# Optimization experiments

Measured on AMD Instinct MI355X. Metric: run time of the kernel, lower is better.

Reference implementation:

```python
import math
import jax, jax.numpy as jnp
import numpy as np

V, D, A, H, FF, L, MD = 500, 512, 512, 8, 2048, 6, 512
HD = A // H
B, S, T = 32, 512, 128


def setup_inputs() -> dict:
    key = jax.random.key(0)
    ks = jax.random.split(key, 40)
    init = lambda k, shape: (jax.random.normal(k, shape, jnp.float32) * 0.02)
    inp = {
        'memory': jax.random.normal(ks[0], (B, S, MD), jnp.float32),
        'memory_lens': jax.random.randint(ks[1], (B,), S // 2, S + 1),
        'ys_in_pad': jax.random.randint(ks[2], (B, T), 0, V),
        'ys_in_lens': jax.random.randint(ks[3], (B,), T // 2, T + 1),
        'emb': init(ks[4], (V, D)),
        'w_out': init(ks[5], (D, V)),
        'b_out': jnp.zeros((V,), jnp.float32),
        # per-layer params stacked on leading L axis (consumed by lax.scan)
        'ln_sa_g': jnp.ones((L, D), jnp.float32), 'ln_sa_b': jnp.zeros((L, D), jnp.float32),
        'sa_wq': init(ks[6], (L, D, A)), 'sa_bq': init(ks[7], (L, A)),
        'sa_wk': init(ks[8], (L, D, A)), 'sa_bk': init(ks[9], (L, A)),
        'sa_wv': init(ks[10], (L, D, A)), 'sa_bv': init(ks[11], (L, A)),
        'sa_wo': init(ks[12], (L, A, D)), 'sa_bo': init(ks[13], (L, D)),
        'ln_ca_g': jnp.ones((L, D), jnp.float32), 'ln_ca_b': jnp.zeros((L, D), jnp.float32),
        'ca_wq': init(ks[14], (L, D, A)), 'ca_bq': init(ks[15], (L, A)),
        'ca_wk': init(ks[16], (L, MD, A)), 'ca_bk': init(ks[17], (L, A)),
        'ca_wv': init(ks[18], (L, MD, A)), 'ca_bv': init(ks[19], (L, A)),
        'ca_wo': init(ks[20], (L, A, D)), 'ca_bo': init(ks[21], (L, D)),
        'ln_ff_g': jnp.ones((L, D), jnp.float32), 'ln_ff_b': jnp.zeros((L, D), jnp.float32),
        'ff_w1': init(ks[22], (L, D, FF)), 'ff_b1': init(ks[23], (L, FF)),
        'ff_w2': init(ks[24], (L, FF, D)), 'ff_b2': init(ks[25], (L, D)),
    }
    return inp


def _layernorm(x, g, b, eps=1e-5):
    m = jnp.mean(x, axis=-1, keepdims=True)
    v = jnp.mean(jnp.square(x - m), axis=-1, keepdims=True)
    return (x - m) * jax.lax.rsqrt(v + eps) * g + b


def _mha(q_in, k_in, v_in, mask, wq, bq, wk, bk, wv, bv, wo, bo):
    # mask: True = disallowed. (B, T, S) for self-attn, (B, 1, S) for cross-attn.
    b_, tq, _ = q_in.shape
    ts = k_in.shape[1]
    q = (q_in @ wq + bq).reshape(b_, tq, H, HD).transpose(0, 2, 1, 3)
    k = (k_in @ wk + bk).reshape(b_, ts, H, HD).transpose(0, 2, 1, 3)
    v = (v_in @ wv + bv).reshape(b_, ts, H, HD).transpose(0, 2, 1, 3)
    s = jnp.einsum('bhtd,bhsd->bhts', q, k) / math.sqrt(HD)
    # penalize_abs_values_gt(limit=50, penalty=1e-4) is identity in the forward
    # pass (it only injects an auxiliary gradient during training).
    s = jnp.where(mask[:, None, :, :], -jnp.inf, s)
    a = jax.nn.softmax(s, axis=-1)  # dropout p=0.0 in this config
    o = jnp.einsum('bhts,bhsd->bhtd', a, v).transpose(0, 2, 1, 3).reshape(b_, tq, A)
    return o @ wo + bo


def _forward(memory, memory_lens, ys_in_pad, ys_in_lens, emb, w_out, b_out, layer_params):
    t = ys_in_pad.shape[1]
    # make_pad_mask | ~subsequent_mask  -> (B, T, T), True = masked
    pad = jnp.arange(t)[None, :] >= ys_in_lens[:, None]            # (B, T)
    causal = ~jnp.tril(jnp.ones((t, t), bool))                     # (T, T)
    tgt_mask = pad[:, None, :] | causal[None]                      # (B, T, T)
    mem_mask = (jnp.arange(memory.shape[1])[None, :] >= memory_lens[:, None])[:, None, :]

    # embedding + sinusoidal positional encoding (dropout in eval = identity)
    pos = jnp.arange(t, dtype=jnp.float32)[:, None]
    div = jnp.exp(jnp.arange(0, D, 2, dtype=jnp.float32) * (-math.log(10000.0) / D))
    pe = jnp.zeros((t, D), jnp.float32)
    pe = pe.at[:, 0::2].set(jnp.sin(pos * div)).at[:, 1::2].set(jnp.cos(pos * div))
    x = emb[ys_in_pad] * math.sqrt(D) + pe[None]

    def step(tgt, p):
        tn = _layernorm(tgt, p['ln_sa_g'], p['ln_sa_b'])
        tgt = tgt + _mha(tn, tn, tn, tgt_mask,
                         p['sa_wq'], p['sa_bq'], p['sa_wk'], p['sa_bk'],
                         p['sa_wv'], p['sa_bv'], p['sa_wo'], p['sa_bo'])
        tn = _layernorm(tgt, p['ln_ca_g'], p['ln_ca_b'])
        tgt = tgt + _mha(tn, memory, memory, mem_mask,
                         p['ca_wq'], p['ca_bq'], p['ca_wk'], p['ca_bk'],
                         p['ca_wv'], p['ca_bv'], p['ca_wo'], p['ca_bo'])
        tn = _layernorm(tgt, p['ln_ff_g'], p['ln_ff_b'])
        h = tn @ p['ff_w1'] + p['ff_b1']
        h = h * jax.nn.sigmoid(h)  # Swish
        tgt = tgt + h @ p['ff_w2'] + p['ff_b2']
        return tgt, None

    x, _ = jax.lax.scan(step, x, layer_params)
    return x @ w_out + b_out  # (B, T, V) logits


_LAYER_KEYS = ['ln_sa_g', 'ln_sa_b', 'sa_wq', 'sa_bq', 'sa_wk', 'sa_bk', 'sa_wv', 'sa_bv',
               'sa_wo', 'sa_bo', 'ln_ca_g', 'ln_ca_b', 'ca_wq', 'ca_bq', 'ca_wk', 'ca_bk',
               'ca_wv', 'ca_bv', 'ca_wo', 'ca_bo', 'ln_ff_g', 'ln_ff_b',
               'ff_w1', 'ff_b1', 'ff_w2', 'ff_b2']


def reference(memory, memory_lens, ys_in_pad, ys_in_lens, emb, w_out, b_out,
              ln_sa_g, ln_sa_b, sa_wq, sa_bq, sa_wk, sa_bk, sa_wv, sa_bv, sa_wo, sa_bo,
              ln_ca_g, ln_ca_b, ca_wq, ca_bq, ca_wk, ca_bk, ca_wv, ca_bv, ca_wo, ca_bo,
              ln_ff_g, ln_ff_b, ff_w1, ff_b1, ff_w2, ff_b2):
    loc = locals()
    layer_params = {k: loc[k] for k in _LAYER_KEYS}
    return _forward(memory, memory_lens, ys_in_pad, ys_in_lens, emb, w_out, b_out, layer_params)
```

## Files before the change

### kernel.cpp

```cpp
#include <hip/hip_runtime.h>
#include <hip/hip_bf16.h>
#include <hip/hip_fp16.h>

constexpr int Bc = 32, Sc = 512, Tc = 128, Dc = 512, Ac = 512, Hc = 8;
constexpr int HDc = 64, FFc = 2048, Lc = 6, Vc = 500;
constexpr int NTOK = Bc * Tc;
constexpr int NMEM = Bc * Sc;

typedef unsigned short u16;
typedef __attribute__((ext_vector_type(8))) short short8;
typedef __attribute__((ext_vector_type(4))) float f32x4;

__device__ __forceinline__ u16 bfc(float x) {
  __hip_bfloat16 h = __float2bfloat16(x);
  return *reinterpret_cast<u16*>(&h);
}

__device__ __forceinline__ void gload16(const void* g, void* l) {
  __builtin_amdgcn_global_load_lds(
      (const __attribute__((address_space(1))) unsigned int*)g,
      (__attribute__((address_space(3))) unsigned int*)l, 16, 0, 0);
}

__device__ __forceinline__ float wave_sum(float v) {
#pragma unroll
  for (int o = 32; o > 0; o >>= 1) v += __shfl_down(v, o);
  return v;
}
__device__ __forceinline__ float wave_max(float v) {
#pragma unroll
  for (int o = 32; o > 0; o >>= 1) v = fmaxf(v, __shfl_down(v, o));
  return v;
}

__global__ __launch_bounds__(256) void embed_pe_k(const int* __restrict__ ys,
                                                  const float* __restrict__ emb,
                                                  float* __restrict__ x) {
  int tok = blockIdx.x;
  int t = tok & (Tc - 1);
  int id = ys[tok];
  int j = threadIdx.x;
  int d0 = 2 * j;
  const float cdiv = -9.210340371976184f / (float)Dc;
  float div = expf((float)d0 * cdiv);
  float ang = (float)t * div;
  float pe0 = sinf(ang), pe1 = cosf(ang);
  const float sc = 22.627416997969522f;
  long base = (long)tok * Dc + d0;
  long ebase = (long)id * Dc + d0;
  x[base]     = emb[ebase]     * sc + pe0;
  x[base + 1] = emb[ebase + 1] * sc + pe1;
}

__global__ __launch_bounds__(256) void layernorm_k(const float* __restrict__ x,
                                                   const float* __restrict__ g,
                                                   const float* __restrict__ bta,
                                                   u16* __restrict__ out) {
  int row = blockIdx.x;
  int tid = threadIdx.x;
  const float* xr = x + (long)row * Dc;
  float2 xv = *(const float2*)(xr + tid * 2);
  __shared__ float red[4];
  float s = wave_sum(xv.x + xv.y);
  if ((tid & 63) == 0) red[tid >> 6] = s;
  __syncthreads();
  float mean = (red[0] + red[1] + red[2] + red[3]) * (1.0f / Dc);
  float dx0 = xv.x - mean, dx1 = xv.y - mean;
  __syncthreads();
  float s2 = wave_sum(dx0 * dx0 + dx1 * dx1);
  if ((tid & 63) == 0) red[tid >> 6] = s2;
  __syncthreads();
  float var = (red[0] + red[1] + red[2] + red[3]) * (1.0f / Dc);
  float rstd = rsqrtf(var + 1e-5f);
  ushort2 o;
  o.x = bfc(dx0 * rstd * g[2 * tid] + bta[2 * tid]);
  o.y = bfc(dx1 * rstd * g[2 * tid + 1] + bta[2 * tid + 1]);
  *(ushort2*)(out + (long)row * Dc + tid * 2) = o;
}

__global__ __launch_bounds__(256) void wtrans_k(const float* __restrict__ src,
                                                u16* __restrict__ dst,
                                                int K, int N, long srcStride, long dstStride) {
  int z = blockIdx.z;
  src += z * srcStride;
  dst += z * dstStride;
  __shared__ float t[32][33];
  int n0 = blockIdx.x * 32, k0 = blockIdx.y * 32;
  int tx = threadIdx.x & 31, ty = threadIdx.x >> 5;
#pragma unroll
  for (int i = 0; i < 4; i++) {
    int n = n0 + tx;
    t[ty + 8 * i][tx] = (n < N) ? src[(long)(k0 + ty + 8 * i) * N + n] : 0.0f;
  }
  __syncthreads();
#pragma unroll
  for (int i = 0; i < 4; i++) {
    dst[(long)(n0 + ty + 8 * i) * K + k0 + tx] = bfc(t[tx][ty + 8 * i]);
  }
}

__global__ __launch_bounds__(256) void f2b_k(const float* __restrict__ in,
                                             u16* __restrict__ out, long n) {
  long i = ((long)blockIdx.x * 256 + threadIdx.x) * 4;
  if (i >= n) return;
  float4 v = *(const float4*)(in + i);
  ushort4 o;
  o.x = bfc(v.x); o.y = bfc(v.y); o.z = bfc(v.z); o.w = bfc(v.w);
  *(ushort4*)(out + i) = o;
}

template <int BMW, int OMODE, bool BIAS, bool RES, bool SWISH, bool NCH>
__global__ __launch_bounds__(256) void mgemm_k(
    const u16* __restrict__ A, const u16* __restrict__ Bt,
    const float* __restrict__ bias0, const float* __restrict__ bias1,
    const float* __restrict__ bias2,
    void* __restrict__ Cv, const float* __restrict__ R,
    int N, int K, int lda, int ldb, int ldc, int nbi,
    long batAo, long batAi, long batBo, long batBi, long batCo, long batCi) {
  constexpr int BM = BMW * 32;
  int z = blockIdx.z;
  int bo = z / nbi, bi = z - bo * nbi;
  const u16* Ab = A + bo * batAo + bi * batAi;
  const u16* Bb = Bt + bo * batBo + bi * batBi;
  long coff = bo * batCo + bi * batCi;
  const float* bias = nullptr;
  if constexpr (BIAS) bias = (bi == 0) ? bias0 : ((bi == 1) ? bias1 : bias2);
  int m0 = blockIdx.y * BM, n0 = blockIdx.x * 128;

  __shared__ __align__(16) u16 As[2][BM * 32];
  __shared__ __align__(16) u16 Bs[2][128 * 32];

  int tid = threadIdx.x;
  int lane = tid & 63, wid = tid >> 6;
  int wm = wid >> 1, wn = wid & 1;
  int fr = lane & 15, grp = lane >> 4;

  f32x4 acc[BMW][4];
#pragma unroll
  for (int i = 0; i < BMW; i++)
#pragma unroll
    for (int j = 0; j < 4; j++) acc[i][j] = (f32x4){0.f, 0.f, 0.f, 0.f};

  const u16* ga = Ab + (long)(m0 + (tid >> 2)) * lda + ((tid & 3) << 3);
  const u16* gb = Bb + (long)(n0 + (tid >> 2)) * ldb + ((tid & 3) << 3);

  auto STAGE = [&](int buf, int kt) {
    u16* lA = &As[buf][tid * 8];
    u16* lB = &Bs[buf][tid * 8];
    gload16(ga + kt, lA);
    if constexpr (BM == 128) gload16(ga + kt + (long)64 * lda, lA + 2048);
    gload16(gb + kt, lB);
    gload16(gb + kt + (long)64 * ldb, lB + 2048);
  };

  auto COMPUTE = [&](int buf) {
    short8 av[BMW], bv[4];
#pragma unroll
    for (int i = 0; i < BMW; i++)
      av[i] = *(const short8*)&As[buf][(wm * BMW * 16 + i * 16 + fr) * 32 + grp * 8];
#pragma unroll
    for (int j = 0; j < 4; j++)
      bv[j] = *(const short8*)&Bs[buf][(wn * 64 + j * 16 + fr) * 32 + grp * 8];
#pragma unroll
    for (int i = 0; i < BMW; i++)
#pragma unroll
      for (int j = 0; j < 4; j++)
        acc[i][j] = __builtin_amdgcn_mfma_f32_16x16x32_bf16(av[i], bv[j], acc[i][j], 0, 0, 0);
  };

  STAGE(0, 0);
  __syncthreads();
  int cur = 0;
  for (int kt = 32; kt < K; kt += 32) {
    STAGE(cur ^ 1, kt);
    COMPUTE(cur);
    __syncthreads();
    cur ^= 1;
  }
  COMPUTE(cur);

  int rbase = m0 + wm * BMW * 16 + grp * 4;
  int cbase = n0 + wn * 64 + fr;
#pragma unroll
  for (int i = 0; i < BMW; i++) {
#pragma unroll
    for (int j = 0; j < 4; j++) {
      int col = cbase + j * 16;
      if (NCH && col >= N) continue;
      float bb = 0.0f;
      if constexpr (BIAS) bb = bias[col];
#pragma unroll
      for (int r = 0; r < 4; r++) {
        int row = rbase + i * 16 + r;
        float v = acc[i][j][r] + bb;
        long idx = coff + (long)row * ldc + col;
        if constexpr (RES) v += R[idx];
        if constexpr (SWISH) v = v / (1.0f + expf(-v));
        if constexpr (OMODE == 0) ((u16*)Cv)[idx] = bfc(v);
        else ((float*)Cv)[idx] = v;
      }
    }
  }
}

template <int SKV, int KVBLK, bool CAUSAL, int IQ>
__global__ __launch_bounds__(256) void fattn_k(
    const u16* __restrict__ Q, const u16* __restrict__ Kg, const u16* __restrict__ Vg,
    u16* __restrict__ O, const int* __restrict__ lens) {
  constexpr int NJ  = KVBLK / 16;
  constexpr int NKV = KVBLK / 32;
  constexpr int NT  = SKV / KVBLK;
  constexpr int KST = 72;
  constexpr int VST = KVBLK + 8;
  constexpr int WR  = 16 * IQ;
  constexpr int WGR = 64 * IQ;
  constexpr int CH  = KVBLK / 32;

  __shared__ __align__(16) u16 Ks[KVBLK * KST];
  __shared__ __align__(16) u16 Vs[64 * VST];
  __shared__ __align__(16) u16 Ps[WGR * VST];

  int bh = blockIdx.x; int b = bh >> 3, h = bh & 7;
  int row00 = blockIdx.y * WGR;
  int tid = threadIdx.x, lane = tid & 63, wid = tid >> 6;
  int fr = lane & 15, grp = lane >> 4;
  int len = lens[b];
  int row0w = row00 + wid * WR;

  short8 qa[IQ][2];
  {
    const u16* qp = Q + ((long)b * Tc + row0w + fr) * 512 + h * 64 + grp * 8;
#pragma unroll
    for (int i = 0; i < IQ; i++)
#pragma unroll
      for (int k2 = 0; k2 < 2; k2++)
        qa[i][k2] = *(const short8*)(qp + (long)i * 16 * 512 + k2 * 32);
  }

  float m_run[IQ][4], l_run[IQ][4];
  f32x4 acc_o[IQ][4];
#pragma unroll
  for (int i = 0; i < IQ; i++)
#pragma unroll
    for (int r = 0; r < 4; r++) { m_run[i][r] = -1e30f; l_run[i][r] = 0.0f; }
#pragma unroll
  for (int i = 0; i < IQ; i++)
#pragma unroll
    for (int j = 0; j < 4; j++) acc_o[i][j] = (f32x4){0.f, 0.f, 0.f, 0.f};

  const u16* Kbase = Kg + ((long)b * SKV) * 512 + h * 64;
  const u16* Vbase = Vg + ((long)b * SKV) * 512 + h * 64;

  int NTeff = NT;
  if constexpr (CAUSAL) NTeff = (row00 + WGR - 1) / KVBLK + 1;
  int lenT = (len + KVBLK - 1) / KVBLK;
  if (lenT < NTeff) NTeff = lenT;

  short8 kreg[CH], vreg[CH];
#pragma unroll
  for (int c = 0; c < CH; c++) {
    int idx = tid + 256 * c; int kv = idx >> 3, s = idx & 7;
    kreg[c] = *(const short8*)(Kbase + (long)kv * 512 + s * 8);
    vreg[c] = *(const short8*)(Vbase + (long)kv * 512 + s * 8);
  }

  for (int t = 0; t < NTeff; t++) {
    int kv0 = t * KVBLK;
    __syncthreads();
#pragma unroll
    for (int c = 0; c < CH; c++) {
      int idx = tid + 256 * c; int kv = idx >> 3, s = idx & 7;
      *(short8*)&Ks[kv * KST + s * 8] = kreg[c];
#pragma unroll
      for (int j = 0; j < 8; j++)
        Vs[(s * 8 + j) * VST + kv] = (u16)vreg[c][j];
    }
    __syncthreads();
    if (t + 1 < NTeff) {
      int kvn = kv0 + KVBLK;
#pragma unroll
      for (int c = 0; c < CH; c++) {
        int idx = tid + 256 * c; int kv = idx >> 3, s = idx & 7;
        kreg[c] = *(const short8*)(Kbase + (long)(kvn + kv) * 512 + s * 8);
        vreg[c] = *(const short8*)(Vbase + (long)(kvn + kv) * 512 + s * 8);
      }
    }

    int jmax = NJ;
    if constexpr (CAUSAL) {
      jmax = (row0w + WR - 1 - kv0) / 16 + 1;
      if (jmax > NJ) jmax = NJ;
    }

    f32x4 accs[IQ][NJ];
#pragma unroll
    for (int j = 0; j < NJ; j++) {
      if (CAUSAL && j >= jmax) continue;
      short8 bv0 = *(const short8*)&Ks[(j * 16 + fr) * KST + grp * 8];
      short8 bv1 = *(const short8*)&Ks[(j * 16 + fr) * KST + 32 + grp * 8];
#pragma unroll
      for (int i = 0; i < IQ; i++) {
        f32x4 a = __builtin_amdgcn_mfma_f32_16x16x32_bf16(qa[i][0], bv0, (f32x4){0.f,0.f,0.f,0.f}, 0, 0, 0);
        accs[i][j] = __builtin_amdgcn_mfma_f32_16x16x32_bf16(qa[i][1], bv1, a, 0, 0, 0);
      }
    }

    float alpha[IQ][4];
#pragma unroll
    for (int i = 0; i < IQ; i++) {
#pragma unroll
      for (int r = 0; r < 4; r++) {
        int qrow = row0w + i * 16 + grp * 4 + r;
        float vmax = -1e30f;
#pragma unroll
        for (int j = 0; j < NJ; j++) {
          if (CAUSAL && j >= jmax) continue;
          int kvb = kv0 + j * 16 + fr;
          float s = accs[i][j][r] * 0.125f;
          bool msk = (kvb >= len) || (CAUSAL && kvb > qrow);
          s = msk ? -1e30f : s;
          accs[i][j][r] = s;
          vmax = fmaxf(vmax, s);
        }
        vmax = fmaxf(vmax, __shfl_xor(vmax, 1));
        vmax = fmaxf(vmax, __shfl_xor(vmax, 2));
        vmax = fmaxf(vmax, __shfl_xor(vmax, 4));
        vmax = fmaxf(vmax, __shfl_xor(vmax, 8));
        float mn = fmaxf(m_run[i][r], vmax);
        float al = __expf(m_run[i][r] - mn);
        m_run[i][r] = mn;
        alpha[i][r] = al;
        float rs = 0.0f;
#pragma unroll
        for (int j = 0; j < NJ; j++) {
          if (CAUSAL && j >= jmax) continue;
          float p = __expf(accs[i][j][r] - mn);
          accs[i][j][r] = p;
          rs += p;
        }
        rs += __shfl_xor(rs, 1);
        rs += __shfl_xor(rs, 2);
        rs += __shfl_xor(rs, 4);
        rs += __shfl_xor(rs, 8);
        l_run[i][r] = l_run[i][r] * al + rs;
      }
    }

#pragma unroll
    for (int i = 0; i < IQ; i++)
#pragma unroll
      for (int j = 0; j < NJ; j++) {
        if (CAUSAL && j >= jmax) continue;
#pragma unroll
        for (int r = 0; r < 4; r++) {
          int prow = wid * WR + i * 16 + grp * 4 + r;
          Ps[prow * VST + j * 16 + fr] = bfc(accs[i][j][r]);
        }
      }

#pragma unroll
    for (int i = 0; i < IQ; i++)
#pragma unroll
      for (int jd = 0; jd < 4; jd++)
#pragma unroll
        for (int r = 0; r < 4; r++)
          acc_o[i][jd][r] *= alpha[i][r];

    int kvmax = NKV;
    if constexpr (CAUSAL) {
      kvmax = (row0w + WR - 1 - kv0) / 32 + 1;
      if (kvmax > NKV) kvmax = NKV;
    }
#pragma unroll
    for (int kk = 0; kk < NKV; kk++) {
      if (CAUSAL && kk >= kvmax) continue;
      short8 pa[IQ];
#pragma unroll
      for (int i = 0; i < IQ; i++)
        pa[i] = *(const short8*)&Ps[(wid * WR + i * 16 + fr) * VST + kk * 32 + grp * 8];
#pragma unroll
      for (int jd = 0; jd < 4; jd++) {
        short8 vb = *(const short8*)&Vs[(jd * 16 + fr) * VST + kk * 32 + grp * 8];
#pragma unroll
        for (int i = 0; i < IQ; i++)
          acc_o[i][jd] = __builtin_amdgcn_mfma_f32_16x16x32_bf16(pa[i], vb, acc_o[i][jd], 0, 0, 0);
      }
    }
  }

#pragma unroll
  for (int i = 0; i < IQ; i++) {
#pragma unroll
    for (int r = 0; r < 4; r++) {
      float inv = 1.0f / l_run[i][r];
      long tok = (long)b * Tc + row0w + i * 16 + grp * 4 + r;
#pragma unroll
      for (int jd = 0; jd < 4; jd++)
        O[tok * 512 + h * 64 + jd * 16 + fr] = bfc(acc_o[i][jd][r] * inv);
    }
  }
}

extern "C" void kernel_launch(void* const* d_in, const int* in_sizes, int n_in,
                              void* d_out, int out_size, void* d_ws, size_t ws_size,
                              hipStream_t stream) {
  const float* memory   = (const float*)d_in[0];
  const int*   mem_lens = (const int*)d_in[1];
  const int*   ys       = (const int*)d_in[2];
  const int*   ys_lens  = (const int*)d_in[3];
  const float* emb      = (const float*)d_in[4];
  const float* w_out    = (const float*)d_in[5];
  const float* b_out    = (const float*)d_in[6];
  const float* pp[26];
  for (int i = 0; i < 26; i++) pp[i] = (const float*)d_in[7 + i];

  constexpr long PLW = 4194304;
  constexpr long OFF_SAQ = 0, OFF_SAK = 262144, OFF_SAV = 524288, OFF_SAO = 786432,
                 OFF_CAQ = 1048576, OFF_CAK = 1310720, OFF_CAV = 1572864,
                 OFF_CAO = 1835008, OFF_FF1 = 2097152, OFF_FF2 = 3145728,
                 OFF_WOUT = 6 * PLW;
  u16*   Wt   = (u16*)d_ws;
  float* X    = (float*)(Wt + 25427968);
  u16*   TO   = (u16*)(X + 2097152);
  u16*   QKV  = TO + 2097152;
  u16*   memb = QKV + 3 * 2097152;
  u16*   Kb   = memb + 8388608;
  u16*   SCR  = Kb + 8388608;
  float* OUT  = (float*)d_out;

  auto WT = [&](const float* src, long dstoff, int K, int N, int Npad, int Lz,
                long srcStride, long dstStride) {
    dim3 g(Npad / 32, K / 32, Lz);
    wtrans_k<<<g, 256, 0, stream>>>(src, Wt + dstoff, K, N, srcStride, dstStride);
  };
  WT(pp[2],  OFF_SAQ, 512, 512, 512, Lc, 262144, PLW);
  WT(pp[4],  OFF_SAK, 512, 512, 512, Lc, 262144, PLW);
  WT(pp[6],  OFF_SAV, 512, 512, 512, Lc, 262144, PLW);
  WT(pp[8],  OFF_SAO, 512, 512, 512, Lc, 262144, PLW);
  WT(pp[12], OFF_CAQ, 512, 512, 512, Lc, 262144, PLW);
  WT(pp[14], OFF_CAK, 512, 512, 512, Lc, 262144, PLW);
  WT(pp[16], OFF_CAV, 512, 512, 512, Lc, 262144, PLW);
  WT(pp[18], OFF_CAO, 512, 512, 512, Lc, 262144, PLW);
  WT(pp[22], OFF_FF1, 512, 2048, 2048, Lc, 1048576, PLW);
  WT(pp[24], OFF_FF2, 2048, 512, 512, Lc, 1048576, PLW);
  WT(w_out,  OFF_WOUT, 512, 500, 512, 1, 0, 0);

  f2b_k<<<(NMEM * Dc / 4 + 255) / 256, 256, 0, stream>>>(memory, memb, (long)NMEM * Dc);
  embed_pe_k<<<NTOK, 256, 0, stream>>>(ys, emb, X);

  for (int l = 0; l < Lc; l++) {
    const u16* WtL = Wt + (long)l * PLW;

    layernorm_k<<<NTOK, 256, 0, stream>>>(X, pp[0] + (long)l * Dc, pp[1] + (long)l * Dc, TO);
    mgemm_k<4, 0, true, false, false, false><<<dim3(4, 32, 3), 256, 0, stream>>>(
        TO, WtL + OFF_SAQ, pp[3] + (long)l * Ac, pp[5] + (long)l * Ac, pp[7] + (long)l * Ac,
        QKV, nullptr, 512, 512, 512, 512, 512, 3, 0, 0, 0, 262144, 0, 2097152);
    fattn_k<128, 128, true, 2><<<dim3(256, 1), 256, 0, stream>>>(
        QKV, QKV + 2097152, QKV + 2 * 2097152, TO, ys_lens);
    mgemm_k<2, 1, true, true, false, false><<<dim3(4, 64, 1), 256, 0, stream>>>(
        TO, WtL + OFF_SAO, pp[9] + (long)l * Dc, nullptr, nullptr, X, X,
        512, 512, 512, 512, 512, 1, 0, 0, 0, 0, 0, 0);

    layernorm_k<<<NTOK, 256, 0, stream>>>(X, pp[10] + (long)l * Dc, pp[11] + (long)l * Dc, TO);
    mgemm_k<2, 0, true, false, false, false><<<dim3(4, 64, 1), 256, 0, stream>>>(
        TO, WtL + OFF_CAQ, pp[13] + (long)l * Ac, nullptr, nullptr, QKV, nullptr,
        512, 512, 512, 512, 512, 1, 0, 0, 0, 0, 0, 0);
    mgemm_k<4, 0, true, false, false, false><<<dim3(4, 128, 2), 256, 0, stream>>>(
        memb, WtL + OFF_CAK, pp[15] + (long)l * Ac, pp[17] + (long)l * Ac, nullptr,
        Kb, nullptr, 512, 512, 512, 512, 512, 2, 0, 0, 0, 262144, 0, 8388608);
    fattn_k<512, 64, false, 1><<<dim3(256, 2), 256, 0, stream>>>(
        QKV, Kb, SCR, TO, mem_lens);
    mgemm_k<2, 1, true, true, false, false><<<dim3(4, 64, 1), 256, 0, stream>>>(
        TO, WtL + OFF_CAO, pp[19] + (long)l * Dc, nullptr, nullptr, X, X,
        512, 512, 512, 512, 512, 1, 0, 0, 0, 0, 0, 0);

    layernorm_k<<<NTOK, 256, 0, stream>>>(X, pp[20] + (long)l * Dc, pp[21] + (long)l * Dc, TO);
    mgemm_k<4, 0, true, false, true, false><<<dim3(16, 32, 1), 256, 0, stream>>>(
        TO, WtL + OFF_FF1, pp[23] + (long)l * FFc, nullptr, nullptr, SCR, nullptr,
        2048, 512, 512, 512, 2048, 1, 0, 0, 0, 0, 0, 0);
    mgemm_k<2, 1, true, true, false, false><<<dim3(4, 64, 1), 256, 0, stream>>>(
        SCR, WtL + OFF_FF2, pp[25] + (long)l * Dc, nullptr, nullptr, X, X,
        512, 2048, 2048, 2048, 512, 1, 0, 0, 0, 0, 0, 0);
  }

  f2b_k<<<(NTOK * Dc / 4 + 255) / 256, 256, 0, stream>>>(X, TO, (long)NTOK * Dc);
  mgemm_k<2, 1, true, false, false, true><<<dim3(4, 64, 1), 256, 0, stream>>>(
      TO, Wt + OFF_WOUT, b_out, nullptr, nullptr, OUT, nullptr,
      500, 512, 512, 512, 500, 1, 0, 0, 0, 0, 0, 0);
}
```

Before: 1.252 ms.

## Skip padded memory rows in KV GEMM, remap blocks across XCDs, batch weight transposes

Several unrelated changes land together. The GEMM kernel remaps workgroup IDs so consecutive tiles share an XCD, and gains an MLEN mode that exits early for memory-row tiles past each batch's memory length in the cross-attention K/V projection. The eight 512x512 weight transposes are merged into one launch, the attention kernel raises wave priority around its MFMA loops, and the cross-attention KV block grows from 64 to 128. Skipped K/V rows are left unwritten, which assumes the attention kernel masks all positions beyond memory_lens.

```diff
diff --git a/kernel.cpp b/kernel.cpp
--- a/kernel.cpp
+++ b/kernel.cpp
@@ -99,6 +99,25 @@
   }
 }
 
+struct PtrPack8 { const float* p[8]; };
+__global__ __launch_bounds__(256) void wtrans8_k(PtrPack8 P, u16* __restrict__ Wt,
+                                                 long PLW) {
+  int z = blockIdx.z;
+  int widx = z / 6, l = z - widx * 6;
+  const float* src = P.p[widx] + (long)l * 262144;
+  u16* dst = Wt + (long)widx * 262144 + (long)l * PLW;
+  __shared__ float t[32][33];
+  int n0 = blockIdx.x * 32, k0 = blockIdx.y * 32;
+  int tx = threadIdx.x & 31, ty = threadIdx.x >> 5;
+#pragma unroll
+  for (int i = 0; i < 4; i++)
+    t[ty + 8 * i][tx] = src[(long)(k0 + ty + 8 * i) * 512 + n0 + tx];
+  __syncthreads();
+#pragma unroll
+  for (int i = 0; i < 4; i++)
+    dst[(long)(n0 + ty + 8 * i) * 512 + k0 + tx] = bfc(t[tx][ty + 8 * i]);
+}
+
 __global__ __launch_bounds__(256) void f2b_k(const float* __restrict__ in,
                                              u16* __restrict__ out, long n) {
   long i = ((long)blockIdx.x * 256 + threadIdx.x) * 4;
@@ -109,23 +128,37 @@
   *(ushort4*)(out + i) = o;
 }
 
-template <int BMW, int OMODE, bool BIAS, bool RES, bool SWISH, bool NCH>
+template <int BMW, int OMODE, bool BIAS, bool RES, bool SWISH, bool NCH, bool MLEN>
 __global__ __launch_bounds__(256) void mgemm_k(
     const u16* __restrict__ A, const u16* __restrict__ Bt,
     const float* __restrict__ bias0, const float* __restrict__ bias1,
     const float* __restrict__ bias2,
-    void* __restrict__ Cv, const float* __restrict__ R,
+    void* __restrict__ Cv, const float* __restrict__ R, const int* __restrict__ mlens,
     int N, int K, int lda, int ldb, int ldc, int nbi,
     long batAo, long batAi, long batBo, long batBi, long batCo, long batCi) {
   constexpr int BM = BMW * 32;
-  int z = blockIdx.z;
+
+  int gx = gridDim.x, gy = gridDim.y;
+  int nwg = gx * gy * gridDim.z;
+  int orig = blockIdx.x + gx * (blockIdx.y + gy * blockIdx.z);
+  int q = nwg >> 3, r = nwg & 7, xcd = orig & 7, off = orig >> 3;
+  int wgid = (xcd < r ? xcd * (q + 1) : r * (q + 1) + (xcd - r) * q) + off;
+  int bxi = wgid % gx; int tmp = wgid / gx;
+  int byi = tmp % gy;  int bzi = tmp / gy;
+
+  int z = bzi;
   int bo = z / nbi, bi = z - bo * nbi;
+  int m0 = byi * BM, n0 = bxi * 128;
+
+  if constexpr (MLEN) {
+    if ((m0 & 511) >= mlens[m0 >> 9]) return;
+  }
+
   const u16* Ab = A + bo * batAo + bi * batAi;
   const u16* Bb = Bt + bo * batBo + bi * batBi;
   long coff = bo * batCo + bi * batCi;
   const float* bias = nullptr;
   if constexpr (BIAS) bias = (bi == 0) ? bias0 : ((bi == 1) ? bias1 : bias2);
-  int m0 = blockIdx.y * BM, n0 = blockIdx.x * 128;
 
   __shared__ __align__(16) u16 As[2][BM * 32];
   __shared__ __align__(16) u16 Bs[2][128 * 32];
@@ -190,9 +223,9 @@
       float bb = 0.0f;
       if constexpr (BIAS) bb = bias[col];
 #pragma unroll
-      for (int r = 0; r < 4; r++) {
-        int row = rbase + i * 16 + r;
-        float v = acc[i][j][r] + bb;
+      for (int r2 = 0; r2 < 4; r2++) {
+        int row = rbase + i * 16 + r2;
+        float v = acc[i][j][r2] + bb;
         long idx = coff + (long)row * ldc + col;
         if constexpr (RES) v += R[idx];
         if constexpr (SWISH) v = v / (1.0f + expf(-v));
@@ -293,6 +326,7 @@
     }
 
     f32x4 accs[IQ][NJ];
+    __builtin_amdgcn_s_setprio(1);
 #pragma unroll
     for (int j = 0; j < NJ; j++) {
       if (CAUSAL && j >= jmax) continue;
@@ -304,6 +338,7 @@
         accs[i][j] = __builtin_amdgcn_mfma_f32_16x16x32_bf16(qa[i][1], bv1, a, 0, 0, 0);
       }
     }
+    __builtin_amdgcn_s_setprio(0);
 
     float alpha[IQ][4];
 #pragma unroll
@@ -371,6 +406,7 @@
       kvmax = (row0w + WR - 1 - kv0) / 32 + 1;
       if (kvmax > NKV) kvmax = NKV;
     }
+    __builtin_amdgcn_s_setprio(1);
 #pragma unroll
     for (int kk = 0; kk < NKV; kk++) {
       if (CAUSAL && kk >= kvmax) continue;
@@ -386,6 +422,7 @@
           acc_o[i][jd] = __builtin_amdgcn_mfma_f32_16x16x32_bf16(pa[i], vb, acc_o[i][jd], 0, 0, 0);
       }
     }
+    __builtin_amdgcn_s_setprio(0);
   }
 
 #pragma unroll
@@ -428,22 +465,13 @@
   u16*   SCR  = Kb + 8388608;
   float* OUT  = (float*)d_out;
 
-  auto WT = [&](const float* src, long dstoff, int K, int N, int Npad, int Lz,
-                long srcStride, long dstStride) {
-    dim3 g(Npad / 32, K / 32, Lz);
-    wtrans_k<<<g, 256, 0, stream>>>(src, Wt + dstoff, K, N, srcStride, dstStride);
-  };
-  WT(pp[2],  OFF_SAQ, 512, 512, 512, Lc, 262144, PLW);
-  WT(pp[4],  OFF_SAK, 512, 512, 512, Lc, 262144, PLW);
-  WT(pp[6],  OFF_SAV, 512, 512, 512, Lc, 262144, PLW);
-  WT(pp[8],  OFF_SAO, 512, 512, 512, Lc, 262144, PLW);
-  WT(pp[12], OFF_CAQ, 512, 512, 512, Lc, 262144, PLW);
-  WT(pp[14], OFF_CAK, 512, 512, 512, Lc, 262144, PLW);
-  WT(pp[16], OFF_CAV, 512, 512, 512, Lc, 262144, PLW);
-  WT(pp[18], OFF_CAO, 512, 512, 512, Lc, 262144, PLW);
-  WT(pp[22], OFF_FF1, 512, 2048, 2048, Lc, 1048576, PLW);
-  WT(pp[24], OFF_FF2, 2048, 512, 512, Lc, 1048576, PLW);
-  WT(w_out,  OFF_WOUT, 512, 500, 512, 1, 0, 0);
+  PtrPack8 P8;
+  P8.p[0] = pp[2];  P8.p[1] = pp[4];  P8.p[2] = pp[6];  P8.p[3] = pp[8];
+  P8.p[4] = pp[12]; P8.p[5] = pp[14]; P8.p[6] = pp[16]; P8.p[7] = pp[18];
+  wtrans8_k<<<dim3(16, 16, 48), 256, 0, stream>>>(P8, Wt, PLW);
+  wtrans_k<<<dim3(64, 16, Lc), 256, 0, stream>>>(pp[22], Wt + OFF_FF1, 512, 2048, 1048576, PLW);
+  wtrans_k<<<dim3(16, 64, Lc), 256, 0, stream>>>(pp[24], Wt + OFF_FF2, 2048, 512, 1048576, PLW);
+  wtrans_k<<<dim3(16, 16, 1), 256, 0, stream>>>(w_out, Wt + OFF_WOUT, 512, 500, 0, 0);
 
   f2b_k<<<(NMEM * Dc / 4 + 255) / 256, 256, 0, stream>>>(memory, memb, (long)NMEM * Dc);
   embed_pe_k<<<NTOK, 256, 0, stream>>>(ys, emb, X);
@@ -452,39 +480,39 @@
     const u16* WtL = Wt + (long)l * PLW;
 
     layernorm_k<<<NTOK, 256, 0, stream>>>(X, pp[0] + (long)l * Dc, pp[1] + (long)l * Dc, TO);
-    mgemm_k<4, 0, true, false, false, false><<<dim3(4, 32, 3), 256, 0, stream>>>(
+    mgemm_k<4, 0, true, false, false, false, false><<<dim3(4, 32, 3), 256, 0, stream>>>(
         TO, WtL + OFF_SAQ, pp[3] + (long)l * Ac, pp[5] + (long)l * Ac, pp[7] + (long)l * Ac,
-        QKV, nullptr, 512, 512, 512, 512, 512, 3, 0, 0, 0, 262144, 0, 2097152);
+        QKV, nullptr, nullptr, 512, 512, 512, 512, 512, 3, 0, 0, 0, 262144, 0, 2097152);
     fattn_k<128, 128, true, 2><<<dim3(256, 1), 256, 0, stream>>>(
         QKV, QKV + 2097152, QKV + 2 * 2097152, TO, ys_lens);
-    mgemm_k<2, 1, true, true, false, false><<<dim3(4, 64, 1), 256, 0, stream>>>(
-        TO, WtL + OFF_SAO, pp[9] + (long)l * Dc, nullptr, nullptr, X, X,
+    mgemm_k<2, 1, true, true, false, false, false><<<dim3(4, 64, 1), 256, 0, stream>>>(
+        TO, WtL + OFF_SAO, pp[9] + (long)l * Dc, nullptr, nullptr, X, X, nullptr,
         512, 512, 512, 512, 512, 1, 0, 0, 0, 0, 0, 0);
 
     layernorm_k<<<NTOK, 256, 0, stream>>>(X, pp[10] + (long)l * Dc, pp[11] + (long)l * Dc, TO);
-    mgemm_k<2, 0, true, false, false, false><<<dim3(4, 64, 1), 256, 0, stream>>>(
-        TO, WtL + OFF_CAQ, pp[13] + (long)l * Ac, nullptr, nullptr, QKV, nullptr,
+    mgemm_k<2, 0, true, false, false, false, false><<<dim3(4, 64, 1), 256, 0, stream>>>(
+        TO, WtL + OFF_CAQ, pp[13] + (long)l * Ac, nullptr, nullptr, QKV, nullptr, nullptr,
         512, 512, 512, 512, 512, 1, 0, 0, 0, 0, 0, 0);
-    mgemm_k<4, 0, true, false, false, false><<<dim3(4, 128, 2), 256, 0, stream>>>(
+    mgemm_k<4, 0, true, false, false, false, true><<<dim3(4, 128, 2), 256, 0, stream>>>(
         memb, WtL + OFF_CAK, pp[15] + (long)l * Ac, pp[17] + (long)l * Ac, nullptr,
-        Kb, nullptr, 512, 512, 512, 512, 512, 2, 0, 0, 0, 262144, 0, 8388608);
-    fattn_k<512, 64, false, 1><<<dim3(256, 2), 256, 0, stream>>>(
+        Kb, nullptr, mem_lens, 512, 512, 512, 512, 512, 2, 0, 0, 0, 262144, 0, 8388608);
+    fattn_k<512, 128, false, 1><<<dim3(256, 2), 256, 0, stream>>>(
         QKV, Kb, SCR, TO, mem_lens);
-    mgemm_k<2, 1, true, true, false, false><<<dim3(4, 64, 1), 256, 0, stream>>>(
-        TO, WtL + OFF_CAO, pp[19] + (long)l * Dc, nullptr, nullptr, X, X,
+    mgemm_k<2, 1, true, true, false, false, false><<<dim3(4, 64, 1), 256, 0, stream>>>(
+        TO, WtL + OFF_CAO, pp[19] + (long)l * Dc, nullptr, nullptr, X, X, nullptr,
         512, 512, 512, 512, 512, 1, 0, 0, 0, 0, 0, 0);
 
     layernorm_k<<<NTOK, 256, 0, stream>>>(X, pp[20] + (long)l * Dc, pp[21] + (long)l * Dc, TO);
-    mgemm_k<4, 0, true, false, true, false><<<dim3(16, 32, 1), 256, 0, stream>>>(
-        TO, WtL + OFF_FF1, pp[23] + (long)l * FFc, nullptr, nullptr, SCR, nullptr,
+    mgemm_k<4, 0, true, false, true, false, false><<<dim3(16, 32, 1), 256, 0, stream>>>(
+        TO, WtL + OFF_FF1, pp[23] + (long)l * FFc, nullptr, nullptr, SCR, nullptr, nullptr,
         2048, 512, 512, 512, 2048, 1, 0, 0, 0, 0, 0, 0);
-    mgemm_k<2, 1, true, true, false, false><<<dim3(4, 64, 1), 256, 0, stream>>>(
-        SCR, WtL + OFF_FF2, pp[25] + (long)l * Dc, nullptr, nullptr, X, X,
+    mgemm_k<2, 1, true, true, false, false, false><<<dim3(4, 64, 1), 256, 0, stream>>>(
+        SCR, WtL + OFF_FF2, pp[25] + (long)l * Dc, nullptr, nullptr, X, X, nullptr,
         512, 2048, 2048, 2048, 512, 1, 0, 0, 0, 0, 0, 0);
   }
 
   f2b_k<<<(NTOK * Dc / 4 + 255) / 256, 256, 0, stream>>>(X, TO, (long)NTOK * Dc);
-  mgemm_k<2, 1, true, false, false, true><<<dim3(4, 64, 1), 256, 0, stream>>>(
-      TO, Wt + OFF_WOUT, b_out, nullptr, nullptr, OUT, nullptr,
+  mgemm_k<2, 1, true, false, false, true, false><<<dim3(4, 64, 1), 256, 0, stream>>>(
+      TO, Wt + OFF_WOUT, b_out, nullptr, nullptr, OUT, nullptr, nullptr,
       500, 512, 512, 512, 500, 1, 0, 0, 0, 0, 0, 0);
 }
```

Result: faster. 1.225 ms (-2.2%).
